# Performance work log

Hardware: AMD Instinct MI355X
Metric: run time of the kernel (lower is better)

## Reference

```python
import jax, jax.numpy as jnp
import numpy as np

EPS = 1e-5
CG_GROUPS = 4
CG_ALPHA = 2.0

def conv3x3(x, w, stride=1):
    # x: [N,C,H,W], w: [O,I,3,3], padding=1
    return jax.lax.conv_general_dilated(
        x, w, window_strides=(stride, stride), padding=((1, 1), (1, 1)),
        dimension_numbers=('NCHW', 'OIHW', 'NCHW'))

def qconv_cg(x, w, theta):
    # Conditional-gated conv (CGNet-style, wbit=abit=32 -> no quantization):
    # base partial sum from first C/cg_groups input channels, remainder gated
    # by soft sigmoid decision on (Yp - per-channel threshold).
    cin = x.shape[1]
    base = cin // CG_GROUPS  # 64 base channels
    yp = conv3x3(x[:, :base], w[:, :base])          # base partial sum [N,O,H,W]
    yr = conv3x3(x[:, base:], w[:, base:])          # remainder partial sum
    d = jax.nn.sigmoid(CG_ALPHA * (yp - theta[None, :, None, None]))
    return yp + d * yr

def bn(x, gamma, beta, mean, var):
    # inference-mode BatchNorm2d
    inv = gamma * jax.lax.rsqrt(var + EPS)
    return x * inv[None, :, None, None] + (beta - mean * inv)[None, :, None, None]

def setup_inputs() -> dict:
    key = jax.random.key(0)
    k0, k1, k2 = jax.random.split(key, 3)
    C = 256
    x = jax.random.normal(k0, (16, C, 56, 56), jnp.float32)
    scale = 1.0 / np.sqrt(C * 9)
    w_a = jax.random.normal(k1, (C, C, 3, 3), jnp.float32) * scale
    w_b = jax.random.normal(k2, (C, C, 3, 3), jnp.float32) * scale
    z = jnp.zeros((C,), jnp.float32)
    o = jnp.ones((C,), jnp.float32)
    return dict(x=x,
                w_a=w_a, theta_a=z, gamma_a=o, beta_a=z, mean_a=z, var_a=o,
                w_b=w_b, theta_b=z, gamma_b=o, beta_b=z, mean_b=z, var_b=o)

def reference(x, w_a, theta_a, gamma_a, beta_a, mean_a, var_a,
              w_b, theta_b, gamma_b, beta_b, mean_b, var_b):
    h = jax.nn.relu(bn(qconv_cg(x, w_a, theta_a), gamma_a, beta_a, mean_a, var_a))
    h = bn(qconv_cg(h, w_b, theta_b), gamma_b, beta_b, mean_b, var_b)
    return jax.nn.relu(x + h)  # identity residual (downsample=None)
```

## Files before the change

### kernel.cpp

```cpp
#include <hip/hip_runtime.h>
#include <hip/hip_bf16.h>
#include <cstdint>
#include <cstddef>


typedef __attribute__((ext_vector_type(8))) short bf16x8;
typedef __attribute__((ext_vector_type(4))) float f32x4;
typedef __attribute__((ext_vector_type(8))) unsigned short u16x8;

#define HP 58
#define WP 58
#define CIN 256
#define NIMG 16

__device__ __forceinline__ unsigned short f2bf(float f) {
  unsigned int u = __float_as_uint(f);
  u += 0x7fffu + ((u >> 16) & 1u);
  return (unsigned short)(u >> 16);
}

#define GLOAD16(gp, lp)                                                        \
  __builtin_amdgcn_global_load_lds(                                            \
      (const __attribute__((address_space(1))) void*)(gp),                     \
      (__attribute__((address_space(3))) void*)(lp), 16, 0, 0)

__global__ void zero_borders(unsigned short* __restrict__ pad) {
  int b = blockIdx.x;
  int img = b / 58, yp = b - img * 58;
  int tid = threadIdx.x;
  u16x8 z = {0, 0, 0, 0, 0, 0, 0, 0};
  unsigned short* row = pad + ((size_t)(img * HP + yp)) * WP * CIN;
  if (yp == 0 || yp == HP - 1) {
    for (int i = tid; i < WP * CIN / 8; i += 256) ((u16x8*)row)[i] = z;
  } else {
    if (tid < 32) ((u16x8*)row)[tid] = z;
    else if (tid < 64) ((u16x8*)row)[(WP - 1) * CIN / 8 + tid - 32] = z;
  }
}

__global__ void prep_w(const float* __restrict__ wa, const float* __restrict__ wb,
                       unsigned short* __restrict__ bta, unsigned short* __restrict__ btb) {
  int id = blockIdx.x * 256 + threadIdx.x;
  const float* w = (id < 65536) ? wa : wb;
  unsigned short* bt = (id < 65536) ? bta : btb;
  int oi = id & 65535;
  int o = oi >> 8, i = oi & 255;
  int cb = i >> 6, c = i & 63;
  float v[9];
#pragma unroll
  for (int t = 0; t < 9; ++t) v[t] = w[(size_t)oi * 9 + t];
#pragma unroll
  for (int t = 0; t < 9; ++t)
    bt[((size_t)((t * 4 + cb) * 256 + o)) * 64 + c] = f2bf(v[t]);
}

__global__ void prep_x(const float* __restrict__ x, unsigned short* __restrict__ xpad) {
  __shared__ float ld[56 * 65];
  int b = blockIdx.x;
  int img = b / 58, y = b - img * 58;
  int tid = threadIdx.x;
  unsigned short* row = xpad + ((size_t)(img * HP + y)) * WP * CIN;
  u16x8 z = {0, 0, 0, 0, 0, 0, 0, 0};
  if (y == 0 || y == HP - 1) {
#pragma unroll
    for (int it = 0; it < 8; ++it) {
      int i = it * 256 + tid;
      if (i < WP * CIN / 8) ((u16x8*)row)[i] = z;
    }
    return;
  }
  if (tid < 32) ((u16x8*)row)[tid] = z;
  else if (tid < 64) ((u16x8*)row)[(WP - 1) * CIN / 8 + tid - 32] = z;
  int ys = y - 1;
  for (int cb = 0; cb < 4; ++cb) {
    __syncthreads();
#pragma unroll
    for (int it = 0; it < 14; ++it) {
      int i = tid + it * 256;
      int cl = i / 56, xx = i - cl * 56;
      ld[xx * 65 + cl] = x[((size_t)(img * 256 + cb * 64 + cl) * 56 + ys) * 56 + xx];
    }
    __syncthreads();
#pragma unroll
    for (int it = 0; it < 14; ++it) {
      int j = tid + it * 256;
      int xx = j >> 6, c = j & 63;
      row[(xx + 1) * CIN + cb * 64 + c] = f2bf(ld[xx * 65 + c]);
    }
  }
}

__device__ __forceinline__ void stage_b(const unsigned short* __restrict__ cbase,
                                        unsigned short* dst, int wid, int lane) {
#pragma unroll
  for (int it = 0; it < 2; ++it) {
    int d = (wid * 2 + it) * 64 + lane;
    int o = d >> 3, s = d & 7;
    const unsigned short* src = cbase + o * 64 + ((s ^ (o & 7)) << 3);
    GLOAD16(src, dst + (wid * 2 + it) * 512);
  }
}

template <int LAYER>
__global__ __launch_bounds__(256, 2)
void conv_cg(const unsigned short* __restrict__ inp,
             const unsigned short* __restrict__ Bt,
             const float* __restrict__ theta,
             const float* __restrict__ gammav,
             const float* __restrict__ betav,
             const float* __restrict__ meanv,
             const float* __restrict__ varv,
             unsigned short* __restrict__ hout,
             const float* __restrict__ xres,
             float* __restrict__ dout)
{
  __shared__ alignas(16) char smem[67584];
  const int tid = threadIdx.x;
  const int lane = tid & 63;
  const int wid = tid >> 6;
  const int l15 = lane & 15, l4 = lane >> 4;

  int bx = blockIdx.x;
  const int oq = bx & 3;
  const int pxg = bx >> 2;
  const int tile = pxg * 4 + wid;
  const int img = tile / 49;
  const int rr = tile - img * 49;
  const int ty = rr / 7, tx = rr - ty * 7;
  const int y0 = ty * 8 + 1, x0 = tx * 8 + 1;
  const size_t img_base = (size_t)img * (HP * WP * CIN);

  unsigned short* sAw = (unsigned short*)smem + wid * 6400;
  unsigned short* sB0 = (unsigned short*)(smem + 51200);
  unsigned short* sB1 = (unsigned short*)(smem + 59392);

  float th[4], sc[4], bi[4];
#pragma unroll
  for (int ni = 0; ni < 4; ++ni) {
    int o = oq * 64 + ni * 16 + l15;
    th[ni] = theta[o];
    float inv = gammav[o] * rsqrtf(varv[o] + 1e-5f);
    sc[ni] = inv;
    bi[ni] = betav[o] - meanv[o] * inv;
  }

  f32x4 acc[4][4], ypv[4][4];
  const f32x4 fzero = {0.f, 0.f, 0.f, 0.f};
#pragma unroll
  for (int i = 0; i < 4; ++i)
#pragma unroll
    for (int j = 0; j < 4; ++j) { acc[i][j] = fzero; ypv[i][j] = fzero; }

  for (int cb = 0; cb < 4; ++cb) {
    {
      const unsigned short* abase = inp + img_base + cb * 64;
#pragma unroll
      for (int it = 0; it < 13; ++it) {
        int v = it * 64 + lane;
        if (v < 800) {
          int ppx = v >> 3, s = v & 7;
          int py = ppx / 10, pxx = ppx - py * 10;
          const unsigned short* src = abase +
              ((size_t)((y0 - 1 + py) * WP + (x0 - 1 + pxx))) * CIN +
              ((s ^ (ppx & 7)) << 3);
          GLOAD16(src, sAw + it * 512);
        }
      }
    }
    stage_b(Bt + ((size_t)((0 * 4 + cb) * 256 + oq * 64)) * 64, sB0, wid, lane);
    __syncthreads();

#pragma unroll
    for (int tap = 0; tap < 9; ++tap) {
      if (tap < 8) {
        unsigned short* nb = ((tap + 1) & 1) ? sB1 : sB0;
        stage_b(Bt + ((size_t)(((tap + 1) * 4 + cb) * 256 + oq * 64)) * 64,
                nb, wid, lane);
      }
      const unsigned short* bb = (tap & 1) ? sB1 : sB0;
      const int dy = tap / 3 - 1, dxx = tap - (tap / 3) * 3 - 1;
#pragma unroll
      for (int ks = 0; ks < 2; ++ks) {
        bf16x8 av[4], bv[4];
#pragma unroll
        for (int mi = 0; mi < 4; ++mi) {
          int ry = mi * 2 + (l15 >> 3);
          int ppx = (ry + dy + 1) * 10 + (l15 & 7) + dxx + 1;
          av[mi] = *(const bf16x8*)(sAw + ppx * 64 +
                                    (((ks * 4 + l4) ^ (ppx & 7)) << 3));
        }
#pragma unroll
        for (int ni = 0; ni < 4; ++ni) {
          int ol = ni * 16 + l15;
          bv[ni] = *(const bf16x8*)(bb + ol * 64 +
                                    (((ks * 4 + l4) ^ (ol & 7)) << 3));
        }
#pragma unroll
        for (int mi = 0; mi < 4; ++mi)
#pragma unroll
          for (int ni = 0; ni < 4; ++ni)
            acc[mi][ni] = __builtin_amdgcn_mfma_f32_16x16x32_bf16(
                av[mi], bv[ni], acc[mi][ni], 0, 0, 0);
      }
      __syncthreads();
    }
    if (cb == 0) {
#pragma unroll
      for (int i = 0; i < 4; ++i)
#pragma unroll
        for (int j = 0; j < 4; ++j) { ypv[i][j] = acc[i][j]; acc[i][j] = fzero; }
    }
  }

  float* sep = (float*)smem + wid * 2176;
#pragma unroll
  for (int r = 0; r < 2; ++r) {
    __syncthreads();
#pragma unroll
    for (int mh = 0; mh < 2; ++mh) {
      int mi = r * 2 + mh;
#pragma unroll
      for (int ni = 0; ni < 4; ++ni)
#pragma unroll
        for (int q = 0; q < 4; ++q) {
          int rowl = mh * 16 + l4 * 4 + q;
          float yp = ypv[mi][ni][q], yr = acc[mi][ni][q];
          float dg = 1.f / (1.f + __expf(-2.f * (yp - th[ni])));
          float v = (yp + dg * yr) * sc[ni] + bi[ni];
          if (LAYER == 1) v = fmaxf(v, 0.f);
          sep[rowl * 68 + ni * 16 + l15] = v;
        }
    }
    __syncthreads();
    if (LAYER == 1) {
#pragma unroll
      for (int it = 0; it < 4; ++it) {
        int u = it * 64 + lane;
        int pxl = u >> 3, s = u & 7;
        int m = r * 32 + pxl;
        int ry = m >> 3, rx = m & 7;
        u16x8 tv;
#pragma unroll
        for (int e = 0; e < 8; ++e) tv[e] = f2bf(sep[pxl * 68 + s * 8 + e]);
        *(u16x8*)(hout + img_base +
                  ((size_t)((y0 + ry) * WP + (x0 + rx))) * CIN + oq * 64 + s * 8) = tv;
      }
    } else {
#pragma unroll
      for (int it = 0; it < 8; ++it) {
        int idx = it * 64 + lane;
        int oc = idx >> 3, t = idx & 7;
        int row4 = t >> 1, half = t & 1;
        int pxl = row4 * 8 + half * 4;
        int gy = y0 - 1 + r * 4 + row4, gx = x0 - 1 + half * 4;
        size_t gb = ((size_t)(img * 256 + oq * 64 + oc) * 56 + gy) * 56 + gx;
        const float4 xa = *(const float4*)(xres + gb);
        float4 o4;
        o4.x = fmaxf(xa.x + sep[(pxl + 0) * 68 + oc], 0.f);
        o4.y = fmaxf(xa.y + sep[(pxl + 1) * 68 + oc], 0.f);
        o4.z = fmaxf(xa.z + sep[(pxl + 2) * 68 + oc], 0.f);
        o4.w = fmaxf(xa.w + sep[(pxl + 3) * 68 + oc], 0.f);
        *(float4*)(dout + gb) = o4;
      }
    }
  }
}

extern "C" void kernel_launch(void* const* d_in, const int* in_sizes, int n_in,
                              void* d_out, int out_size, void* d_ws, size_t ws_size,
                              hipStream_t stream) {
  const float* x    = (const float*)d_in[0];
  const float* w_a  = (const float*)d_in[1];
  const float* th_a = (const float*)d_in[2];
  const float* ga_a = (const float*)d_in[3];
  const float* be_a = (const float*)d_in[4];
  const float* mu_a = (const float*)d_in[5];
  const float* va_a = (const float*)d_in[6];
  const float* w_b  = (const float*)d_in[7];
  const float* th_b = (const float*)d_in[8];
  const float* ga_b = (const float*)d_in[9];
  const float* be_b = (const float*)d_in[10];
  const float* mu_b = (const float*)d_in[11];
  const float* va_b = (const float*)d_in[12];
  float* out = (float*)d_out;

  char* ws = (char*)d_ws;
  unsigned short* xpad = (unsigned short*)ws;
  unsigned short* hpad = (unsigned short*)(ws + 27558912);
  unsigned short* bta  = (unsigned short*)(ws + 2 * 27558912);
  unsigned short* btb  = (unsigned short*)(ws + 2 * 27558912 + 1179648);
  (void)ws_size; (void)in_sizes; (void)n_in; (void)out_size;

  hipLaunchKernelGGL(zero_borders, dim3(NIMG * HP), dim3(256), 0, stream, hpad);
  hipLaunchKernelGGL(prep_w, dim3(512), dim3(256), 0, stream, w_a, w_b, bta, btb);
  hipLaunchKernelGGL(prep_x, dim3(NIMG * HP), dim3(256), 0, stream, x, xpad);

  hipLaunchKernelGGL((conv_cg<1>), dim3(784), dim3(256), 0, stream,
                     xpad, bta, th_a, ga_a, be_a, mu_a, va_a,
                     hpad, (const float*)nullptr, (float*)nullptr);
  hipLaunchKernelGGL((conv_cg<2>), dim3(784), dim3(256), 0, stream,
                     hpad, btb, th_b, ga_b, be_b, mu_b, va_b,
                     (unsigned short*)nullptr, x, out);
}
```

Before: 320.6 us.

## Share input tile across warps per block, stream weights from global into registers

Changes the block decomposition so that one block covers one 8x8 pixel tile and all 256 output channels, with each warp owning 64 output channels. The shared input tile is double-buffered in LDS across channel blocks, and weights are loaded straight from global memory into registers with tap-level double buffering, replacing the LDS staging of B. It also remaps block indices across images, cuts LDS use and removes most per-tap barriers. The cost is a higher register load and weight reads that now go through global or L2 memory instead of LDS.

```diff
diff --git a/kernel.cpp b/kernel.cpp
--- a/kernel.cpp
+++ b/kernel.cpp
@@ -87,17 +87,6 @@
       int xx = j >> 6, c = j & 63;
       row[(xx + 1) * CIN + cb * 64 + c] = f2bf(ld[xx * 65 + c]);
     }
-  }
-}
-
-__device__ __forceinline__ void stage_b(const unsigned short* __restrict__ cbase,
-                                        unsigned short* dst, int wid, int lane) {
-#pragma unroll
-  for (int it = 0; it < 2; ++it) {
-    int d = (wid * 2 + it) * 64 + lane;
-    int o = d >> 3, s = d & 7;
-    const unsigned short* src = cbase + o * 64 + ((s ^ (o & 7)) << 3);
-    GLOAD16(src, dst + (wid * 2 + it) * 512);
   }
 }
 
@@ -114,108 +103,127 @@
              const float* __restrict__ xres,
              float* __restrict__ dout)
 {
-  __shared__ alignas(16) char smem[67584];
+  __shared__ alignas(16) char smem[34816];
+  unsigned short* sA0 = (unsigned short*)smem;
+  unsigned short* sA1 = (unsigned short*)(smem + 12800);
+
   const int tid = threadIdx.x;
   const int lane = tid & 63;
   const int wid = tid >> 6;
   const int l15 = lane & 15, l4 = lane >> 4;
 
   int bx = blockIdx.x;
-  const int oq = bx & 3;
-  const int pxg = bx >> 2;
-  const int tile = pxg * 4 + wid;
-  const int img = tile / 49;
-  const int rr = tile - img * 49;
+  bx = (bx & 7) * 98 + (bx >> 3);
+  const int img = bx / 49;
+  const int rr = bx - img * 49;
   const int ty = rr / 7, tx = rr - ty * 7;
   const int y0 = ty * 8 + 1, x0 = tx * 8 + 1;
   const size_t img_base = (size_t)img * (HP * WP * CIN);
-
-  unsigned short* sAw = (unsigned short*)smem + wid * 6400;
-  unsigned short* sB0 = (unsigned short*)(smem + 51200);
-  unsigned short* sB1 = (unsigned short*)(smem + 59392);
-
+  const unsigned short* acorner =
+      inp + img_base + ((size_t)((y0 - 1) * WP + (x0 - 1))) * CIN;
+
+  int srcoff[4];
+#pragma unroll
+  for (int it = 0; it < 4; ++it) {
+    int u = it * 256 + tid;
+    int ppx = u >> 3, s = u & 7;
+    int py = ppx / 10, pxx = ppx - py * 10;
+    srcoff[it] = (py * WP + pxx) * CIN + ((s ^ (ppx & 7)) << 3);
+  }
+  const int blane = l15 * 64 + l4 * 8;
+  const unsigned short* Bw = Bt + (size_t)wid * 64 * 64;
+
+  f32x4 acc[4][4], ypv[4][4];
+  const f32x4 fzero = {0.f, 0.f, 0.f, 0.f};
+#pragma unroll
+  for (int i = 0; i < 4; ++i)
+#pragma unroll
+    for (int j = 0; j < 4; ++j) { acc[i][j] = fzero; ypv[i][j] = fzero; }
+
+  auto stageA = [&](unsigned short* buf, int cb) {
+#pragma unroll
+    for (int it = 0; it < 4; ++it) {
+      if (it * 256 + tid < 800)
+        GLOAD16(acorner + cb * 64 + srcoff[it], buf + (it * 256 + wid * 64) * 8);
+    }
+  };
+  auto loadB = [&](bf16x8 (&dst)[4][2], int tapcb) {
+    const unsigned short* bb = Bw + (size_t)tapcb * 16384 + blane;
+#pragma unroll
+    for (int ni = 0; ni < 4; ++ni)
+#pragma unroll
+      for (int ks = 0; ks < 2; ++ks)
+        dst[ni][ks] = *(const bf16x8*)(bb + ni * 1024 + ks * 32);
+  };
+  auto doTap = [&](const unsigned short* sAb, bf16x8 (&B)[4][2], int dy, int dxx) {
+#pragma unroll
+    for (int ks = 0; ks < 2; ++ks) {
+      bf16x8 av[4];
+#pragma unroll
+      for (int mi = 0; mi < 4; ++mi) {
+        int ppx = (mi * 2 + (l15 >> 3) + dy + 1) * 10 + (l15 & 7) + dxx + 1;
+        av[mi] = *(const bf16x8*)(sAb + ppx * 64 +
+                                  (((ks * 4 + l4) ^ (ppx & 7)) << 3));
+      }
+#pragma unroll
+      for (int mi = 0; mi < 4; ++mi)
+#pragma unroll
+        for (int ni = 0; ni < 4; ++ni)
+          acc[mi][ni] = __builtin_amdgcn_mfma_f32_16x16x32_bf16(
+              av[mi], B[ni][ks], acc[mi][ni], 0, 0, 0);
+    }
+  };
+
+  bf16x8 bb0[4][2], bb1[4][2];
+  stageA(sA0, 0);
+  loadB(bb0, 0);
+  asm volatile("s_waitcnt vmcnt(8)" ::: "memory");
+  __builtin_amdgcn_s_barrier();
+  __builtin_amdgcn_sched_barrier(0);
+
+#pragma unroll
+  for (int cb = 0; cb < 4; ++cb) {
+    unsigned short* sCur = (cb & 1) ? sA1 : sA0;
+    unsigned short* sNxt = (cb & 1) ? sA0 : sA1;
+    if (cb < 3) stageA(sNxt, cb + 1);
+#pragma unroll
+    for (int tap = 0; tap < 9; ++tap) {
+      const int dy = tap / 3 - 1, dxx = tap % 3 - 1;
+      const int ntap = (tap < 8) ? tap + 1 : 0;
+      const int ncb = (tap < 8) ? cb : cb + 1;
+      if (!(cb == 3 && tap == 8)) {
+        if (((cb + tap) & 1) == 0) loadB(bb1, ntap * 4 + ncb);
+        else                       loadB(bb0, ntap * 4 + ncb);
+      }
+      if (((cb + tap) & 1) == 0) doTap(sCur, bb0, dy, dxx);
+      else                       doTap(sCur, bb1, dy, dxx);
+    }
+    if (cb < 3) {
+      asm volatile("s_waitcnt vmcnt(8)" ::: "memory");
+      __builtin_amdgcn_s_barrier();
+      __builtin_amdgcn_sched_barrier(0);
+    }
+    if (cb == 0) {
+#pragma unroll
+      for (int i = 0; i < 4; ++i)
+#pragma unroll
+        for (int j = 0; j < 4; ++j) { ypv[i][j] = acc[i][j]; acc[i][j] = fzero; }
+    }
+  }
+  __syncthreads();
+
+  float* sep = (float*)smem + wid * 2176;
   float th[4], sc[4], bi[4];
 #pragma unroll
   for (int ni = 0; ni < 4; ++ni) {
-    int o = oq * 64 + ni * 16 + l15;
+    int o = wid * 64 + ni * 16 + l15;
     th[ni] = theta[o];
     float inv = gammav[o] * rsqrtf(varv[o] + 1e-5f);
     sc[ni] = inv;
     bi[ni] = betav[o] - meanv[o] * inv;
   }
-
-  f32x4 acc[4][4], ypv[4][4];
-  const f32x4 fzero = {0.f, 0.f, 0.f, 0.f};
-#pragma unroll
-  for (int i = 0; i < 4; ++i)
-#pragma unroll
-    for (int j = 0; j < 4; ++j) { acc[i][j] = fzero; ypv[i][j] = fzero; }
-
-  for (int cb = 0; cb < 4; ++cb) {
-    {
-      const unsigned short* abase = inp + img_base + cb * 64;
-#pragma unroll
-      for (int it = 0; it < 13; ++it) {
-        int v = it * 64 + lane;
-        if (v < 800) {
-          int ppx = v >> 3, s = v & 7;
-          int py = ppx / 10, pxx = ppx - py * 10;
-          const unsigned short* src = abase +
-              ((size_t)((y0 - 1 + py) * WP + (x0 - 1 + pxx))) * CIN +
-              ((s ^ (ppx & 7)) << 3);
-          GLOAD16(src, sAw + it * 512);
-        }
-      }
-    }
-    stage_b(Bt + ((size_t)((0 * 4 + cb) * 256 + oq * 64)) * 64, sB0, wid, lane);
-    __syncthreads();
-
-#pragma unroll
-    for (int tap = 0; tap < 9; ++tap) {
-      if (tap < 8) {
-        unsigned short* nb = ((tap + 1) & 1) ? sB1 : sB0;
-        stage_b(Bt + ((size_t)(((tap + 1) * 4 + cb) * 256 + oq * 64)) * 64,
-                nb, wid, lane);
-      }
-      const unsigned short* bb = (tap & 1) ? sB1 : sB0;
-      const int dy = tap / 3 - 1, dxx = tap - (tap / 3) * 3 - 1;
-#pragma unroll
-      for (int ks = 0; ks < 2; ++ks) {
-        bf16x8 av[4], bv[4];
-#pragma unroll
-        for (int mi = 0; mi < 4; ++mi) {
-          int ry = mi * 2 + (l15 >> 3);
-          int ppx = (ry + dy + 1) * 10 + (l15 & 7) + dxx + 1;
-          av[mi] = *(const bf16x8*)(sAw + ppx * 64 +
-                                    (((ks * 4 + l4) ^ (ppx & 7)) << 3));
-        }
-#pragma unroll
-        for (int ni = 0; ni < 4; ++ni) {
-          int ol = ni * 16 + l15;
-          bv[ni] = *(const bf16x8*)(bb + ol * 64 +
-                                    (((ks * 4 + l4) ^ (ol & 7)) << 3));
-        }
-#pragma unroll
-        for (int mi = 0; mi < 4; ++mi)
-#pragma unroll
-          for (int ni = 0; ni < 4; ++ni)
-            acc[mi][ni] = __builtin_amdgcn_mfma_f32_16x16x32_bf16(
-                av[mi], bv[ni], acc[mi][ni], 0, 0, 0);
-      }
-      __syncthreads();
-    }
-    if (cb == 0) {
-#pragma unroll
-      for (int i = 0; i < 4; ++i)
-#pragma unroll
-        for (int j = 0; j < 4; ++j) { ypv[i][j] = acc[i][j]; acc[i][j] = fzero; }
-    }
-  }
-
-  float* sep = (float*)smem + wid * 2176;
 #pragma unroll
   for (int r = 0; r < 2; ++r) {
-    __syncthreads();
 #pragma unroll
     for (int mh = 0; mh < 2; ++mh) {
       int mi = r * 2 + mh;
@@ -231,7 +239,6 @@
           sep[rowl * 68 + ni * 16 + l15] = v;
         }
     }
-    __syncthreads();
     if (LAYER == 1) {
 #pragma unroll
       for (int it = 0; it < 4; ++it) {
@@ -243,7 +250,7 @@
 #pragma unroll
         for (int e = 0; e < 8; ++e) tv[e] = f2bf(sep[pxl * 68 + s * 8 + e]);
         *(u16x8*)(hout + img_base +
-                  ((size_t)((y0 + ry) * WP + (x0 + rx))) * CIN + oq * 64 + s * 8) = tv;
+                  ((size_t)((y0 + ry) * WP + (x0 + rx))) * CIN + wid * 64 + s * 8) = tv;
       }
     } else {
 #pragma unroll
@@ -253,7 +260,7 @@
         int row4 = t >> 1, half = t & 1;
         int pxl = row4 * 8 + half * 4;
         int gy = y0 - 1 + r * 4 + row4, gx = x0 - 1 + half * 4;
-        size_t gb = ((size_t)(img * 256 + oq * 64 + oc) * 56 + gy) * 56 + gx;
+        size_t gb = ((size_t)(img * 256 + wid * 64 + oc) * 56 + gy) * 56 + gx;
         const float4 xa = *(const float4*)(xres + gb);
         float4 o4;
         o4.x = fmaxf(xa.x + sep[(pxl + 0) * 68 + oc], 0.f);
```

Result: slower. 463.2 us (+44.5%).

## Restructure conv to 4-row full-channel tiles with double-buffered A/B staging

Applied to the files above, without the earlier changes.

Each 512-thread block now computes 4 full image rows for all 256 output channels, with an 8-wave 2x4 layout. Each wave holds 112 pixels x 64 channels of accumulators. Input halo tiles and weight chunks are double-buffered in 152KB of LDS, using explicit vmcnt waits, raw barriers and setprio so loads overlap the MFMA work. The base partial sum is kept packed as bf16 to save registers. The launch drops to 224 blocks, which may underfill the GPU, and the bf16 rounding of yp adds a small accuracy risk.

```diff
diff --git a/kernel.cpp b/kernel.cpp
--- a/kernel.cpp
+++ b/kernel.cpp
@@ -13,6 +13,10 @@
 #define CIN 256
 #define NIMG 16
 
+#define A_BUF 45056
+#define B0_OFF 90112
+#define B1_OFF 122880
+
 __device__ __forceinline__ unsigned short f2bf(float f) {
   unsigned int u = __float_as_uint(f);
   u += 0x7fffu + ((u >> 16) & 1u);
@@ -23,6 +27,10 @@
   __builtin_amdgcn_global_load_lds(                                            \
       (const __attribute__((address_space(1))) void*)(gp),                     \
       (__attribute__((address_space(3))) void*)(lp), 16, 0, 0)
+#define GLOAD4(gp, lp)                                                         \
+  __builtin_amdgcn_global_load_lds(                                            \
+      (const __attribute__((address_space(1))) void*)(gp),                     \
+      (__attribute__((address_space(3))) void*)(lp), 4, 0, 0)
 
 __global__ void zero_borders(unsigned short* __restrict__ pad) {
   int b = blockIdx.x;
@@ -90,19 +98,8 @@
   }
 }
 
-__device__ __forceinline__ void stage_b(const unsigned short* __restrict__ cbase,
-                                        unsigned short* dst, int wid, int lane) {
-#pragma unroll
-  for (int it = 0; it < 2; ++it) {
-    int d = (wid * 2 + it) * 64 + lane;
-    int o = d >> 3, s = d & 7;
-    const unsigned short* src = cbase + o * 64 + ((s ^ (o & 7)) << 3);
-    GLOAD16(src, dst + (wid * 2 + it) * 512);
-  }
-}
-
 template <int LAYER>
-__global__ __launch_bounds__(256, 2)
+__global__ __launch_bounds__(512, 2)
 void conv_cg(const unsigned short* __restrict__ inp,
              const unsigned short* __restrict__ Bt,
              const float* __restrict__ theta,
@@ -114,153 +111,219 @@
              const float* __restrict__ xres,
              float* __restrict__ dout)
 {
-  __shared__ alignas(16) char smem[67584];
+  __shared__ alignas(16) char smem[155648];
+
   const int tid = threadIdx.x;
   const int lane = tid & 63;
   const int wid = tid >> 6;
+  const int wm = wid >> 2, wn = wid & 3;
   const int l15 = lane & 15, l4 = lane >> 4;
 
   int bx = blockIdx.x;
-  const int oq = bx & 3;
-  const int pxg = bx >> 2;
-  const int tile = pxg * 4 + wid;
-  const int img = tile / 49;
-  const int rr = tile - img * 49;
-  const int ty = rr / 7, tx = rr - ty * 7;
-  const int y0 = ty * 8 + 1, x0 = tx * 8 + 1;
+  int sw = (bx & 7) * 28 + (bx >> 3);
+  const int img = sw / 14, rg = sw - img * 14;
   const size_t img_base = (size_t)img * (HP * WP * CIN);
-
-  unsigned short* sAw = (unsigned short*)smem + wid * 6400;
-  unsigned short* sB0 = (unsigned short*)(smem + 51200);
-  unsigned short* sB1 = (unsigned short*)(smem + 59392);
-
+  const char* inb = (const char*)(inp + img_base);
+  const char* Btb = (const char*)Bt;
+
+  int a16off[5];
+#pragma unroll
+  for (int it = 0; it < 5; ++it) {
+    int u = it * 512 + tid;
+    int p = u >> 3, s = u & 7;
+    int pr = p / 58, pc = p - pr * 58;
+    a16off[it] = (((rg * 4 + pr) * 58) + pc) * 512 + ((s ^ (p & 7)) << 4);
+  }
+  int a4off[2];
+#pragma unroll
+  for (int it = 0; it < 2; ++it) {
+    int j = it * 512 + tid;
+    int jc = j > 895 ? 895 : j;
+    int bb = 40960 + jc * 4;
+    int p = bb >> 7;
+    int pr = p / 58, pc = p - pr * 58;
+    a4off[it] = (((rg * 4 + pr) * 58) + pc) * 512 +
+                ((((bb >> 4) & 7) ^ (p & 7)) << 4) + (bb & 15);
+  }
+  int boff[4];
+#pragma unroll
+  for (int it = 0; it < 4; ++it) {
+    int u = it * 512 + tid;
+    int o = u >> 3, s = u & 7;
+    boff[it] = o * 128 + ((s ^ (o & 7)) << 4);
+  }
+  int pb[7];
+#pragma unroll
+  for (int mi = 0; mi < 7; ++mi) {
+    int pl = mi * 16 + l15;
+    int ar = pl / 56, ac = pl - ar * 56;
+    pb[mi] = (wm * 2 + ar + 1) * 58 + ac + 1;
+  }
+  int ro128[4], rx7[4];
+#pragma unroll
+  for (int ni = 0; ni < 4; ++ni) {
+    int ro = wn * 64 + ni * 16 + l15;
+    ro128[ni] = ro << 7;
+    rx7[ni] = ro & 7;
+  }
+
+  auto stageA = [&](int abuf, int cb) {
+    const char* s0 = inb + cb * 128;
+#pragma unroll
+    for (int it = 0; it < 5; ++it)
+      GLOAD16(s0 + a16off[it], smem + abuf + it * 8192 + wid * 1024);
+#pragma unroll
+    for (int it = 0; it < 2; ++it)
+      GLOAD4(s0 + a4off[it], smem + abuf + 40960 + it * 2048 + wid * 256);
+  };
+  auto stageB = [&](int bbuf, int chunk) {
+    const char* s0 = Btb + (size_t)chunk * 32768;
+#pragma unroll
+    for (int it = 0; it < 4; ++it)
+      GLOAD16(s0 + boff[it], smem + bbuf + it * 8192 + wid * 1024);
+  };
+
+  f32x4 acc[7][4];
+  unsigned int ypk[7][4][2];
+  const f32x4 fzero = {0.f, 0.f, 0.f, 0.f};
+#pragma unroll
+  for (int i = 0; i < 7; ++i)
+#pragma unroll
+    for (int j = 0; j < 4; ++j) acc[i][j] = fzero;
+
+  stageA(0, 0);
+  stageB(B0_OFF, 0);
+
+  for (int cb = 0; cb < 4; ++cb) {
+    const char* Abp = smem + ((cb & 1) ? A_BUF : 0);
+    const int An = (cb & 1) ? 0 : A_BUF;
+#pragma unroll
+    for (int tap = 0; tap < 9; ++tap) {
+      const int dy = tap / 3 - 1, dxx = tap % 3 - 1;
+      const char* Bcp = smem + (((cb + tap) & 1) ? B1_OFF : B0_OFF);
+      const int Bn = ((cb + tap) & 1) ? B0_OFF : B1_OFF;
+      if (tap < 8)       stageB(Bn, (tap + 1) * 4 + cb);
+      else if (cb < 3)   stageB(Bn, 0 * 4 + (cb + 1));
+      if (tap == 0 && cb < 3) stageA(An, cb + 1);
+      if (cb == 3 && tap == 8)
+        asm volatile("s_waitcnt vmcnt(0)" ::: "memory");
+      else if (tap <= 1 && cb < 3)
+        asm volatile("s_waitcnt vmcnt(11)" ::: "memory");
+      else
+        asm volatile("s_waitcnt vmcnt(4)" ::: "memory");
+      __builtin_amdgcn_s_barrier();
+      __builtin_amdgcn_s_setprio(1);
+#pragma unroll
+      for (int ks = 0; ks < 2; ++ks) {
+        bf16x8 av[7], bv[4];
+#pragma unroll
+        for (int mi = 0; mi < 7; ++mi) {
+          int p = pb[mi] + dy * 58 + dxx;
+          av[mi] = *(const bf16x8*)(Abp + p * 128 +
+                                    (((ks * 4 + l4) ^ (p & 7)) << 4));
+        }
+#pragma unroll
+        for (int ni = 0; ni < 4; ++ni)
+          bv[ni] = *(const bf16x8*)(Bcp + ro128[ni] +
+                                    (((ks * 4 + l4) ^ rx7[ni]) << 4));
+#pragma unroll
+        for (int mi = 0; mi < 7; ++mi)
+#pragma unroll
+          for (int ni = 0; ni < 4; ++ni)
+            acc[mi][ni] = __builtin_amdgcn_mfma_f32_16x16x32_bf16(
+                av[mi], bv[ni], acc[mi][ni], 0, 0, 0);
+      }
+      __builtin_amdgcn_s_setprio(0);
+      __builtin_amdgcn_s_barrier();
+    }
+    if (cb == 0) {
+#pragma unroll
+      for (int mi = 0; mi < 7; ++mi)
+#pragma unroll
+        for (int ni = 0; ni < 4; ++ni) {
+          ypk[mi][ni][0] = (unsigned int)f2bf(acc[mi][ni][0]) |
+                           ((unsigned int)f2bf(acc[mi][ni][1]) << 16);
+          ypk[mi][ni][1] = (unsigned int)f2bf(acc[mi][ni][2]) |
+                           ((unsigned int)f2bf(acc[mi][ni][3]) << 16);
+          acc[mi][ni] = fzero;
+        }
+    }
+  }
+
+  char* slice = smem + wid * 19456;
   float th[4], sc[4], bi[4];
 #pragma unroll
   for (int ni = 0; ni < 4; ++ni) {
-    int o = oq * 64 + ni * 16 + l15;
+    int o = wn * 64 + ni * 16 + l15;
     th[ni] = theta[o];
     float inv = gammav[o] * rsqrtf(varv[o] + 1e-5f);
     sc[ni] = inv;
     bi[ni] = betav[o] - meanv[o] * inv;
   }
 
-  f32x4 acc[4][4], ypv[4][4];
-  const f32x4 fzero = {0.f, 0.f, 0.f, 0.f};
-#pragma unroll
-  for (int i = 0; i < 4; ++i)
-#pragma unroll
-    for (int j = 0; j < 4; ++j) { acc[i][j] = fzero; ypv[i][j] = fzero; }
-
-  for (int cb = 0; cb < 4; ++cb) {
-    {
-      const unsigned short* abase = inp + img_base + cb * 64;
-#pragma unroll
-      for (int it = 0; it < 13; ++it) {
-        int v = it * 64 + lane;
-        if (v < 800) {
-          int ppx = v >> 3, s = v & 7;
-          int py = ppx / 10, pxx = ppx - py * 10;
-          const unsigned short* src = abase +
-              ((size_t)((y0 - 1 + py) * WP + (x0 - 1 + pxx))) * CIN +
-              ((s ^ (ppx & 7)) << 3);
-          GLOAD16(src, sAw + it * 512);
-        }
-      }
-    }
-    stage_b(Bt + ((size_t)((0 * 4 + cb) * 256 + oq * 64)) * 64, sB0, wid, lane);
-    __syncthreads();
-
-#pragma unroll
-    for (int tap = 0; tap < 9; ++tap) {
-      if (tap < 8) {
-        unsigned short* nb = ((tap + 1) & 1) ? sB1 : sB0;
-        stage_b(Bt + ((size_t)(((tap + 1) * 4 + cb) * 256 + oq * 64)) * 64,
-                nb, wid, lane);
-      }
-      const unsigned short* bb = (tap & 1) ? sB1 : sB0;
-      const int dy = tap / 3 - 1, dxx = tap - (tap / 3) * 3 - 1;
-#pragma unroll
-      for (int ks = 0; ks < 2; ++ks) {
-        bf16x8 av[4], bv[4];
-#pragma unroll
-        for (int mi = 0; mi < 4; ++mi) {
-          int ry = mi * 2 + (l15 >> 3);
-          int ppx = (ry + dy + 1) * 10 + (l15 & 7) + dxx + 1;
-          av[mi] = *(const bf16x8*)(sAw + ppx * 64 +
-                                    (((ks * 4 + l4) ^ (ppx & 7)) << 3));
-        }
-#pragma unroll
-        for (int ni = 0; ni < 4; ++ni) {
-          int ol = ni * 16 + l15;
-          bv[ni] = *(const bf16x8*)(bb + ol * 64 +
-                                    (((ks * 4 + l4) ^ (ol & 7)) << 3));
-        }
-#pragma unroll
-        for (int mi = 0; mi < 4; ++mi)
-#pragma unroll
-          for (int ni = 0; ni < 4; ++ni)
-            acc[mi][ni] = __builtin_amdgcn_mfma_f32_16x16x32_bf16(
-                av[mi], bv[ni], acc[mi][ni], 0, 0, 0);
-      }
-      __syncthreads();
-    }
-    if (cb == 0) {
-#pragma unroll
-      for (int i = 0; i < 4; ++i)
-#pragma unroll
-        for (int j = 0; j < 4; ++j) { ypv[i][j] = acc[i][j]; acc[i][j] = fzero; }
-    }
-  }
-
-  float* sep = (float*)smem + wid * 2176;
-#pragma unroll
-  for (int r = 0; r < 2; ++r) {
-    __syncthreads();
-#pragma unroll
-    for (int mh = 0; mh < 2; ++mh) {
-      int mi = r * 2 + mh;
+  if (LAYER == 1) {
+#pragma unroll
+    for (int mi = 0; mi < 7; ++mi)
 #pragma unroll
       for (int ni = 0; ni < 4; ++ni)
 #pragma unroll
         for (int q = 0; q < 4; ++q) {
-          int rowl = mh * 16 + l4 * 4 + q;
-          float yp = ypv[mi][ni][q], yr = acc[mi][ni][q];
+          int pl = mi * 16 + l4 * 4 + q;
+          unsigned int pk = ypk[mi][ni][q >> 1];
+          float yp = __uint_as_float((q & 1) ? (pk & 0xffff0000u) : (pk << 16));
+          float yr = acc[mi][ni][q];
           float dg = 1.f / (1.f + __expf(-2.f * (yp - th[ni])));
-          float v = (yp + dg * yr) * sc[ni] + bi[ni];
-          if (LAYER == 1) v = fmaxf(v, 0.f);
-          sep[rowl * 68 + ni * 16 + l15] = v;
-        }
-    }
-    __syncthreads();
-    if (LAYER == 1) {
-#pragma unroll
-      for (int it = 0; it < 4; ++it) {
-        int u = it * 64 + lane;
-        int pxl = u >> 3, s = u & 7;
-        int m = r * 32 + pxl;
-        int ry = m >> 3, rx = m & 7;
-        u16x8 tv;
-#pragma unroll
-        for (int e = 0; e < 8; ++e) tv[e] = f2bf(sep[pxl * 68 + s * 8 + e]);
-        *(u16x8*)(hout + img_base +
-                  ((size_t)((y0 + ry) * WP + (x0 + rx))) * CIN + oq * 64 + s * 8) = tv;
-      }
-    } else {
-#pragma unroll
-      for (int it = 0; it < 8; ++it) {
-        int idx = it * 64 + lane;
-        int oc = idx >> 3, t = idx & 7;
-        int row4 = t >> 1, half = t & 1;
-        int pxl = row4 * 8 + half * 4;
-        int gy = y0 - 1 + r * 4 + row4, gx = x0 - 1 + half * 4;
-        size_t gb = ((size_t)(img * 256 + oq * 64 + oc) * 56 + gy) * 56 + gx;
-        const float4 xa = *(const float4*)(xres + gb);
-        float4 o4;
-        o4.x = fmaxf(xa.x + sep[(pxl + 0) * 68 + oc], 0.f);
-        o4.y = fmaxf(xa.y + sep[(pxl + 1) * 68 + oc], 0.f);
-        o4.z = fmaxf(xa.z + sep[(pxl + 2) * 68 + oc], 0.f);
-        o4.w = fmaxf(xa.w + sep[(pxl + 3) * 68 + oc], 0.f);
-        *(float4*)(dout + gb) = o4;
+          float v = fmaxf((yp + dg * yr) * sc[ni] + bi[ni], 0.f);
+          *(unsigned short*)(slice + pl * 144 + (ni * 16 + l15) * 2) = f2bf(v);
+        }
+#pragma unroll
+    for (int it = 0; it < 14; ++it) {
+      int j = it * 64 + lane;
+      int pl = j >> 3, s = j & 7;
+      int lr = pl / 56, xc = pl - lr * 56;
+      int gy = rg * 4 + wm * 2 + lr + 1, gx = xc + 1;
+      u16x8 tv = *(const u16x8*)(slice + pl * 144 + s * 16);
+      *(u16x8*)(hout + img_base + ((size_t)(gy * WP + gx)) * CIN +
+                wn * 64 + s * 8) = tv;
+    }
+  } else {
+#pragma unroll
+    for (int r2 = 0; r2 < 2; ++r2) {
+#pragma unroll
+      for (int mi = 0; mi < 7; ++mi)
+#pragma unroll
+        for (int nh = 0; nh < 2; ++nh) {
+          int ni = r2 * 2 + nh;
+#pragma unroll
+          for (int q = 0; q < 4; ++q) {
+            int pl = mi * 16 + l4 * 4 + q;
+            unsigned int pk = ypk[mi][ni][q >> 1];
+            float yp = __uint_as_float((q & 1) ? (pk & 0xffff0000u) : (pk << 16));
+            float yr = acc[mi][ni][q];
+            float dg = 1.f / (1.f + __expf(-2.f * (yp - th[ni])));
+            float v = (yp + dg * yr) * sc[ni] + bi[ni];
+            *(float*)(slice + (nh * 16 + l15) * 464 + pl * 4) = v;
+          }
+        }
+#pragma unroll
+      for (int it = 0; it < 16; ++it) {
+        int j = it * 64 + lane;
+        int r = j >> 4, x4 = j & 15;
+        if (x4 < 14) {
+          int o_loc = r >> 1, yl = r & 1;
+          int oc = wn * 64 + r2 * 32 + o_loc;
+          int gy = rg * 4 + wm * 2 + yl;
+          size_t gb = ((size_t)(img * 256 + oc) * 56 + gy) * 56 + x4 * 4;
+          const float4 xa = *(const float4*)(xres + gb);
+          const float4 hv = *(const float4*)(slice + o_loc * 464 +
+                                             (yl * 56 + x4 * 4) * 4);
+          float4 o4;
+          o4.x = fmaxf(xa.x + hv.x, 0.f);
+          o4.y = fmaxf(xa.y + hv.y, 0.f);
+          o4.z = fmaxf(xa.z + hv.z, 0.f);
+          o4.w = fmaxf(xa.w + hv.w, 0.f);
+          *(float4*)(dout + gb) = o4;
+        }
       }
     }
   }
@@ -295,10 +358,10 @@
   hipLaunchKernelGGL(prep_w, dim3(512), dim3(256), 0, stream, w_a, w_b, bta, btb);
   hipLaunchKernelGGL(prep_x, dim3(NIMG * HP), dim3(256), 0, stream, x, xpad);
 
-  hipLaunchKernelGGL((conv_cg<1>), dim3(784), dim3(256), 0, stream,
+  hipLaunchKernelGGL((conv_cg<1>), dim3(NIMG * 14), dim3(512), 0, stream,
                      xpad, bta, th_a, ga_a, be_a, mu_a, va_a,
                      hpad, (const float*)nullptr, (float*)nullptr);
-  hipLaunchKernelGGL((conv_cg<2>), dim3(784), dim3(256), 0, stream,
+  hipLaunchKernelGGL((conv_cg<2>), dim3(NIMG * 14), dim3(512), 0, stream,
                      hpad, btb, th_b, ga_b, be_b, mu_b, va_b,
                      (unsigned short*)nullptr, x, out);
 }
```

After: 617.9 us. +92.7%, slower.
